# Kernel tuning notes

Measured on AMD Instinct MI355X. Metric: run time of the kernel, lower is better.

The kernel has to match this reference:

```python
import jax, jax.numpy as jnp
import numpy as np

B, S, HIDDEN, NH = 2, 2048, 1024, 16
D = HIDDEN // NH  # 64
PHYS_W, CONS_W = 0.2, 0.15
LN_EPS = 1e-5


def _layernorm(x, gamma, beta):
    mu = jnp.mean(x, axis=-1, keepdims=True)
    var = jnp.mean(jnp.square(x - mu), axis=-1, keepdims=True)
    return (x - mu) * jax.lax.rsqrt(var + LN_EPS) * gamma + beta


def setup_inputs() -> dict:
    key = jax.random.key(0)
    ks = jax.random.split(key, 12)
    s = 0.02
    return {
        "cnn_features": jax.random.normal(ks[0], (B, S, HIDDEN), jnp.float32),
        "llm_features": jax.random.normal(ks[1], (B, S, HIDDEN), jnp.float32),
        # Linear weights stored [in, out] so y = x @ W + b (torch's W.T)
        "Wq": jax.random.normal(ks[2], (HIDDEN, HIDDEN), jnp.float32) * s,
        "bq": jnp.zeros((HIDDEN,), jnp.float32),
        "Wk": jax.random.normal(ks[3], (HIDDEN, HIDDEN), jnp.float32) * s,
        "bk": jnp.zeros((HIDDEN,), jnp.float32),
        "Wv": jax.random.normal(ks[4], (HIDDEN, HIDDEN), jnp.float32) * s,
        "bv": jnp.zeros((HIDDEN,), jnp.float32),
        "Wo": jax.random.normal(ks[5], (HIDDEN, HIDDEN), jnp.float32) * s,
        "bo": jnp.zeros((HIDDEN,), jnp.float32),
        "energy_emb": jax.random.normal(ks[6], (1, 1, HIDDEN), jnp.float32),
        "mass_emb": jax.random.normal(ks[7], (1, 1, HIDDEN), jnp.float32),
        "momentum_emb": jax.random.normal(ks[8], (1, 1, HIDDEN), jnp.float32),
        "gamma": jnp.ones((HIDDEN,), jnp.float32),
        "beta": jnp.zeros((HIDDEN,), jnp.float32),
    }


def reference(cnn_features, llm_features, Wq, bq, Wk, bk, Wv, bv, Wo, bo,
              energy_emb, mass_emb, momentum_emb, gamma, beta):
    Bsz, Sc, _ = cnn_features.shape
    Sl = llm_features.shape[1]

    def attn(q_in, kv_in):
        Sq, Sk = q_in.shape[1], kv_in.shape[1]
        Q = (q_in @ Wq + bq).reshape(Bsz, Sq, NH, D).transpose(0, 2, 1, 3)   # bhqd
        K = (kv_in @ Wk + bk).reshape(Bsz, Sk, NH, D).transpose(0, 2, 1, 3)  # bhkd
        V = (kv_in @ Wv + bv).reshape(Bsz, Sk, NH, D).transpose(0, 2, 1, 3)  # bhkd
        scores = jnp.einsum('bhqd,bhkd->bhqk', Q, K) / np.float32(np.sqrt(D))
        # physics biases: require Sq == Sk (elementwise Q*K), shape [B,H,Sq,1]
        energy_bias = jnp.sum(Q * K, axis=-1, keepdims=True) * PHYS_W
        mass_bias = jnp.mean(Q + K, axis=-1, keepdims=True) * CONS_W
        attn_w = jax.nn.softmax(scores + energy_bias + mass_bias, axis=-1)
        attended = jnp.einsum('bhqk,bhkd->bhqd', attn_w, V)
        attended = attended.transpose(0, 2, 1, 3).reshape(Bsz, Sq, HIDDEN)
        out = attended @ Wo + bo
        return _layernorm(q_in + out, gamma, beta)

    phys = jnp.concatenate([
        jnp.broadcast_to(energy_emb, (Bsz, 1, HIDDEN)),
        jnp.broadcast_to(mass_emb, (Bsz, 1, HIDDEN)),
        jnp.broadcast_to(momentum_emb, (Bsz, 1, HIDDEN)),
    ], axis=1)  # [B, 3, HIDDEN]
    aug_cnn = jnp.concatenate([cnn_features, phys], axis=1)  # [B, Sc+3, H]
    aug_llm = jnp.concatenate([llm_features, phys], axis=1)  # [B, Sl+3, H]

    cnn_att = attn(aug_cnn, aug_llm)
    llm_att = attn(aug_llm, aug_cnn)
    return cnn_att[:, :Sc, :], llm_att[:, :Sl, :]
```

## Files before the change

### kernel.cpp

```cpp
#include <hip/hip_runtime.h>

#define BN 2
#define SS 2048
#define SA 2051
#define HID 1024
#define NHD 16
#define DH 64
#define GSTR 40
#define VTLD 8320
#define KSTR 72
#define VSTR 40
#define MFMA16 __builtin_amdgcn_mfma_f32_16x16x32_bf16
#define QSCALE 0.18033688011112042f

typedef __attribute__((ext_vector_type(4))) float floatx4;
typedef __attribute__((ext_vector_type(8))) short bf16x8;
typedef __attribute__((ext_vector_type(2))) unsigned uintx2;

__device__ __forceinline__ float bf2f(short s) {
  union { unsigned u; float f; } v; v.u = ((unsigned)(unsigned short)s) << 16; return v.f;
}
__device__ __forceinline__ short f2bf(float f) {
  union { float f; unsigned u; } v; v.f = f;
  unsigned u = v.u;
  u += 0x7FFF + ((u >> 16) & 1);
  return (short)(u >> 16);
}
__device__ __forceinline__ unsigned pack2(float lo, float hi) {
  unsigned ul = __float_as_uint(lo) + 0x8000u;
  unsigned uh = __float_as_uint(hi) + 0x8000u;
  return __builtin_amdgcn_perm(uh, ul, 0x07060302u);
}
__device__ __forceinline__ unsigned cvtpk(float lo, float hi) {
  unsigned r;
  asm("v_cvt_pk_bf16_f32 %0, %1, %2" : "=v"(r) : "v"(lo), "v"(hi));
  return r;
}
__device__ __forceinline__ uintx2 qtrans(unsigned A, unsigned B) {
  auto t = __builtin_amdgcn_permlane32_swap(A, B, false, false);
  auto u = __builtin_amdgcn_permlane16_swap(t[0], t[1], false, false);
  uintx2 r; r[0] = u[0]; r[1] = u[1];
  return r;
}
__device__ __forceinline__ bool in_is_f32(const unsigned* graw) {
  return graw[0] == 0x3F800000u;
}

__global__ __launch_bounds__(256) void convert_in(const void* __restrict__ src, long off,
                                                  short* __restrict__ dst, int n,
                                                  const unsigned* __restrict__ graw) {
  bool f32 = in_is_f32(graw);
  int i = (blockIdx.x * 256 + threadIdx.x) * 4;
  int stride = gridDim.x * 1024;
  if (f32) {
    const float* s = (const float*)src + off;
    for (; i < n; i += stride) {
      float4 v = *(const float4*)(s + i);
      short4 o; o.x = f2bf(v.x); o.y = f2bf(v.y); o.z = f2bf(v.z); o.w = f2bf(v.w);
      *(short4*)(dst + i) = o;
    }
  } else {
    const short* s = (const short*)src + off;
    for (; i < n; i += stride)
      *(short4*)(dst + i) = *(const short4*)(s + i);
  }
}

__global__ __launch_bounds__(256) void convert_small(
    const void* s0, const void* s1, const void* s2, const void* s3,
    const void* s4, const void* s5, const void* s6, const void* s7,
    const void* s8, short* __restrict__ dst, const unsigned* __restrict__ graw) {
  bool f32 = in_is_f32(graw);
  const void* srcs[9] = {s0, s1, s2, s3, s4, s5, s6, s7, s8};
  const void* s = srcs[blockIdx.x];
  short* d = dst + (size_t)blockIdx.x * 1024;
  for (int i = threadIdx.x; i < 1024; i += 256)
    d[i] = f32 ? f2bf(((const float*)s)[i]) : ((const short*)s)[i];
}

__global__ __launch_bounds__(256) void conv_wt(const void* __restrict__ W,
    short* __restrict__ WT, const unsigned* __restrict__ graw) {
  __shared__ short tile[32][33];
  bool f32 = in_is_f32(graw);
  int n0 = blockIdx.x * 32, k0 = blockIdx.y * 32;
  int tx = threadIdx.x & 31, ty = threadIdx.x >> 5;
#pragma unroll
  for (int i = 0; i < 4; i++) {
    int k = k0 + ty + i*8;
    short v = f32 ? f2bf(((const float*)W)[(size_t)k * HID + n0 + tx])
                  : ((const short*)W)[(size_t)k * HID + n0 + tx];
    tile[ty + i*8][tx] = v;
  }
  __syncthreads();
#pragma unroll
  for (int i = 0; i < 4; i++)
    WT[(size_t)(n0 + ty + i*8) * HID + k0 + tx] = tile[tx][ty + i*8];
}

__global__ __launch_bounds__(256) void gemm_bf(
    const short* __restrict__ A, int tailA,
    const short* __restrict__ B, int tailB,
    const short* __restrict__ embB,
    const short* __restrict__ bias, int bias_row, float scale,
    short* __restrict__ out16, float* __restrict__ out32, long ldc,
    const void* __restrict__ rc0, const void* __restrict__ rc1,
    const unsigned* __restrict__ graw) {
  __shared__ __align__(16) short sA[128 * GSTR];
  __shared__ __align__(16) short sB[128 * GSTR];
  int t = threadIdx.x;
  int wave = t >> 6, lane = t & 63, l16 = lane & 15, quad = lane >> 4;
  int m0 = blockIdx.y * 128, n0 = blockIdx.x * 128;
  int msub = (wave >> 1) * 64, nsub = (wave & 1) * 64;

  floatx4 acc[4][4] = {};
  for (int k0 = 0; k0 < HID; k0 += 32) {
    bf16x8 av[2], bv2[2];
#pragma unroll
    for (int rep = 0; rep < 2; rep++) {
      int cid = rep * 256 + t;
      int row = cid >> 2, kc = (cid & 3) * 8;
      int ra = m0 + row;
      const short* ap;
      if (tailA && ra >= 8192) ap = embB + (size_t)((ra > 8194 ? 8194 : ra) - 8192) * 1024;
      else                     ap = A + (size_t)ra * HID;
      av[rep] = *(const bf16x8*)(ap + k0 + kc);
      int rb = n0 + row;
      const short* bp;
      if (tailB && rb >= 8192) bp = embB + (size_t)((rb > 8194 ? 8194 : rb) - 8192) * 1024;
      else                     bp = B + (size_t)rb * HID;
      bv2[rep] = *(const bf16x8*)(bp + k0 + kc);
    }
    __syncthreads();
#pragma unroll
    for (int rep = 0; rep < 2; rep++) {
      int cid = rep * 256 + t;
      int row = cid >> 2, kc = (cid & 3) * 8;
      *(bf16x8*)(&sA[row * GSTR + kc]) = av[rep];
      *(bf16x8*)(&sB[row * GSTR + kc]) = bv2[rep];
    }
    __syncthreads();
    bf16x8 af[4], bf_[4];
#pragma unroll
    for (int i = 0; i < 4; i++) {
      af[i]  = *(const bf16x8*)(&sA[(msub + i*16 + l16) * GSTR + quad*8]);
      bf_[i] = *(const bf16x8*)(&sB[(nsub + i*16 + l16) * GSTR + quad*8]);
    }
#pragma unroll
    for (int mi = 0; mi < 4; mi++)
#pragma unroll
      for (int ni = 0; ni < 4; ni++)
        acc[mi][ni] = MFMA16(af[mi], bf_[ni], acc[mi][ni], 0, 0, 0);
  }

  bool f32in = in_is_f32(graw);
#pragma unroll
  for (int mi = 0; mi < 4; mi++)
#pragma unroll
    for (int ni = 0; ni < 4; ni++) {
      int col = n0 + nsub + ni*16 + l16;
      float bcol = bias_row ? 0.f : bf2f(bias[col]);
#pragma unroll
      for (int r = 0; r < 4; r++) {
        int m = m0 + msub + mi*16 + quad*4 + r;
        float v = (acc[mi][ni][r] + (bias_row ? bf2f(bias[m]) : bcol)) * scale;
        if (out32) {
          float res;
          if (f32in) res = ((const float*)(m < 4096 ? rc0 : rc1))[(size_t)(m & 4095) * HID + col];
          else       res = bf2f(((const short*)(m < 4096 ? rc0 : rc1))[(size_t)(m & 4095) * HID + col]);
          out32[(size_t)m * HID + col] = v + res;
        } else {
          out16[(size_t)m * ldc + col] = f2bf(v);
        }
      }
    }
}

__global__ __launch_bounds__(256, 4) void flash3(
    const short* __restrict__ Qa, const short* __restrict__ Ka,
    const short* __restrict__ VTa, short* __restrict__ att) {
  __shared__ __align__(16) short sK0[32*KSTR], sK1[32*KSTR];
  __shared__ __align__(16) short sV0[64*VSTR], sV1[64*VSTR];
  int t = threadIdx.x, wave = t >> 6, lane = t & 63;
  int l16 = lane & 15, quad = lane >> 4;
  int bid = blockIdx.x;
  int swz = (bid & 7) * 128 + (bid >> 3);
  int qt  = swz & 15;
  int h   = (swz >> 4) & 15;
  int sb  = swz >> 8;
  int side = sb >> 1, b = sb & 1;
  int qrow0 = side * 4096 + b * 2048;
  int kvb = (side ^ 1) * 4096 + b * 2048;
  int q0 = qt * 128 + wave * 32;

  const short* qp0 = Qa + (size_t)(qrow0 + q0 + l16) * HID + h*DH + quad*8;
  const short* qp1 = qp0 + 16 * HID;
  bf16x8 qa0 = *(const bf16x8*)qp0, qb0 = *(const bf16x8*)(qp0 + 32);
  bf16x8 qa1 = *(const bf16x8*)qp1, qb1 = *(const bf16x8*)(qp1 + 32);

  float rs0 = 0.f, rs1 = 0.f;
  floatx4 oA[4] = {}, oB[4] = {};

  int krow = t >> 3, kc8 = (t & 7) * 8;
  int vrow = t >> 2, vc8 = (t & 3) * 8;
  const short* kgp = Ka + (size_t)(kvb + krow) * HID + h*DH + kc8;
  const short* vgp = VTa + (size_t)(h*DH + vrow) * VTLD + kvb + vc8;
  bf16x8 kreg = *(const bf16x8*)kgp;
  bf16x8 vreg = *(const bf16x8*)vgp;
  short *kw = sK0, *vw = sV0, *ka = sK1, *va = sV1;

  for (int kv0 = 0; kv0 < 2048; kv0 += 32) {
    *(bf16x8*)(kw + krow*KSTR + kc8) = kreg;
    *(bf16x8*)(vw + vrow*VSTR + vc8) = vreg;
    __syncthreads();
    kgp += 32*HID; vgp += 32;
    kreg = *(const bf16x8*)kgp;
    vreg = *(const bf16x8*)vgp;

    bf16x8 k00 = *(const bf16x8*)(kw + l16*KSTR + quad*8);
    bf16x8 k01 = *(const bf16x8*)(kw + l16*KSTR + 32 + quad*8);
    bf16x8 k10 = *(const bf16x8*)(kw + (16 + l16)*KSTR + quad*8);
    bf16x8 k11 = *(const bf16x8*)(kw + (16 + l16)*KSTR + 32 + quad*8);
    bf16x8 v0 = *(const bf16x8*)(vw + l16*VSTR + quad*8);
    bf16x8 v1 = *(const bf16x8*)(vw + (16 + l16)*VSTR + quad*8);
    bf16x8 v2 = *(const bf16x8*)(vw + (32 + l16)*VSTR + quad*8);
    bf16x8 v3 = *(const bf16x8*)(vw + (48 + l16)*VSTR + quad*8);

    floatx4 s00 = {}, s10 = {}, s01 = {}, s11 = {};
    s00 = MFMA16(k00, qa0, s00, 0, 0, 0); s00 = MFMA16(k01, qb0, s00, 0, 0, 0);
    s10 = MFMA16(k10, qa0, s10, 0, 0, 0); s10 = MFMA16(k11, qb0, s10, 0, 0, 0);
    s01 = MFMA16(k00, qa1, s01, 0, 0, 0); s01 = MFMA16(k01, qb1, s01, 0, 0, 0);
    s11 = MFMA16(k10, qa1, s11, 0, 0, 0); s11 = MFMA16(k11, qb1, s11, 0, 0, 0);

    floatx4 p00, p10, p01, p11;
#pragma unroll
    for (int r = 0; r < 4; r++) {
      p00[r] = exp2f(s00[r]); p10[r] = exp2f(s10[r]);
      p01[r] = exp2f(s01[r]); p11[r] = exp2f(s11[r]);
    }
    rs0 += ((p00[0]+p00[1])+(p00[2]+p00[3])) + ((p10[0]+p10[1])+(p10[2]+p10[3]));
    rs1 += ((p01[0]+p01[1])+(p01[2]+p01[3])) + ((p11[0]+p11[1])+(p11[2]+p11[3]));

    unsigned pc00 = cvtpk(p00[0], p00[1]), pc01 = cvtpk(p00[2], p00[3]);
    unsigned pc10 = cvtpk(p10[0], p10[1]), pc11 = cvtpk(p10[2], p10[3]);
    unsigned pd00 = cvtpk(p01[0], p01[1]), pd01 = cvtpk(p01[2], p01[3]);
    unsigned pd10 = cvtpk(p11[0], p11[1]), pd11 = cvtpk(p11[2], p11[3]);
    uintx2 uA0 = qtrans(pc00, pc10);
    uintx2 uA1 = qtrans(pc01, pc11);
    uintx2 uB0 = qtrans(pd00, pd10);
    uintx2 uB1 = qtrans(pd01, pd11);
    union { unsigned u[4]; bf16x8 v; } pf0, pf1;
    pf0.u[0] = uA0[0]; pf0.u[1] = uA1[0]; pf0.u[2] = uA0[1]; pf0.u[3] = uA1[1];
    pf1.u[0] = uB0[0]; pf1.u[1] = uB1[0]; pf1.u[2] = uB0[1]; pf1.u[3] = uB1[1];

    oA[0] = MFMA16(v0, pf0.v, oA[0], 0, 0, 0);
    oA[1] = MFMA16(v1, pf0.v, oA[1], 0, 0, 0);
    oA[2] = MFMA16(v2, pf0.v, oA[2], 0, 0, 0);
    oA[3] = MFMA16(v3, pf0.v, oA[3], 0, 0, 0);
    oB[0] = MFMA16(v0, pf1.v, oB[0], 0, 0, 0);
    oB[1] = MFMA16(v1, pf1.v, oB[1], 0, 0, 0);
    oB[2] = MFMA16(v2, pf1.v, oB[2], 0, 0, 0);
    oB[3] = MFMA16(v3, pf1.v, oB[3], 0, 0, 0);

    short* tk = kw; kw = ka; ka = tk;
    short* tv = vw; vw = va; va = tv;
  }

  {
    int er = l16 < 2 ? l16 : 2;
    const short* kpt = Ka + (size_t)(8192 + er) * HID + h*DH + quad*8;
    bf16x8 tk0 = *(const bf16x8*)kpt;
    bf16x8 tk1 = *(const bf16x8*)(kpt + 32);
    floatx4 s00 = {}, s01 = {};
    s00 = MFMA16(tk0, qa0, s00, 0, 0, 0); s00 = MFMA16(tk1, qb0, s00, 0, 0, 0);
    s01 = MFMA16(tk0, qa1, s01, 0, 0, 0); s01 = MFMA16(tk1, qb1, s01, 0, 0, 0);
    floatx4 p00, p01;
#pragma unroll
    for (int r = 0; r < 4; r++) {
      bool val = (quad == 0) && (r < 3);
      p00[r] = val ? exp2f(s00[r]) : 0.f;
      p01[r] = val ? exp2f(s01[r]) : 0.f;
    }
    rs0 += (p00[0]+p00[1]) + (p00[2]+p00[3]);
    rs1 += (p01[0]+p01[1]) + (p01[2]+p01[3]);
    unsigned pc00 = cvtpk(p00[0], p00[1]), pc01 = cvtpk(p00[2], p00[3]);
    unsigned pd00 = cvtpk(p01[0], p01[1]), pd01 = cvtpk(p01[2], p01[3]);
    uintx2 uA0 = qtrans(pc00, 0u);
    uintx2 uA1 = qtrans(pc01, 0u);
    uintx2 uB0 = qtrans(pd00, 0u);
    uintx2 uB1 = qtrans(pd01, 0u);
    union { unsigned u[4]; bf16x8 v; } pf0, pf1;
    pf0.u[0] = uA0[0]; pf0.u[1] = uA1[0]; pf0.u[2] = uA0[1]; pf0.u[3] = uA1[1];
    pf1.u[0] = uB0[0]; pf1.u[1] = uB1[0]; pf1.u[2] = uB0[1]; pf1.u[3] = uB1[1];
    const short* vtp = VTa + (size_t)(h*DH + l16) * VTLD + 8192 + quad*8;
    bf16x8 v0 = *(const bf16x8*)vtp;
    bf16x8 v1 = *(const bf16x8*)(vtp + 16*VTLD);
    bf16x8 v2 = *(const bf16x8*)(vtp + 32*VTLD);
    bf16x8 v3 = *(const bf16x8*)(vtp + 48*VTLD);
    oA[0] = MFMA16(v0, pf0.v, oA[0], 0, 0, 0);
    oA[1] = MFMA16(v1, pf0.v, oA[1], 0, 0, 0);
    oA[2] = MFMA16(v2, pf0.v, oA[2], 0, 0, 0);
    oA[3] = MFMA16(v3, pf0.v, oA[3], 0, 0, 0);
    oB[0] = MFMA16(v0, pf1.v, oB[0], 0, 0, 0);
    oB[1] = MFMA16(v1, pf1.v, oB[1], 0, 0, 0);
    oB[2] = MFMA16(v2, pf1.v, oB[2], 0, 0, 0);
    oB[3] = MFMA16(v3, pf1.v, oB[3], 0, 0, 0);
  }

  rs0 += __shfl_xor(rs0, 16, 64); rs0 += __shfl_xor(rs0, 32, 64);
  rs1 += __shfl_xor(rs1, 16, 64); rs1 += __shfl_xor(rs1, 32, 64);
  float i0 = 1.f / rs0, i1 = 1.f / rs1;

  unsigned* ob0 = (unsigned*)(att + (size_t)(qrow0 + q0 + l16) * HID + h*DH + quad*4);
  unsigned* ob1 = (unsigned*)(att + (size_t)(qrow0 + q0 + 16 + l16) * HID + h*DH + quad*4);
#pragma unroll
  for (int n = 0; n < 4; n++) {
    ob0[n*8]     = pack2(oA[n][0]*i0, oA[n][1]*i0);
    ob0[n*8 + 1] = pack2(oA[n][2]*i0, oA[n][3]*i0);
    ob1[n*8]     = pack2(oB[n][0]*i1, oB[n][1]*i1);
    ob1[n*8 + 1] = pack2(oB[n][2]*i1, oB[n][3]*i1);
  }
}

__global__ __launch_bounds__(256) void ln_kernel(
    const float* __restrict__ y, const short* __restrict__ gamma,
    const short* __restrict__ beta, void* __restrict__ outp, long orow,
    const unsigned* __restrict__ graw) {
  bool f32o = in_is_f32(graw);
  int row = blockIdx.x;
  int t = threadIdx.x;
  const float* yr = y + (size_t)row * HID;
  float4 v = ((const float4*)yr)[t];
  float sum = v.x + v.y + v.z + v.w;
#pragma unroll
  for (int off = 32; off >= 1; off >>= 1) sum += __shfl_xor(sum, off, 64);
  __shared__ float red[8];
  int wave = t >> 6, lane = t & 63;
  if (lane == 0) red[wave] = sum;
  __syncthreads();
  float mu = (red[0] + red[1] + red[2] + red[3]) * (1.f/HID);
  float dx = v.x - mu, dy = v.y - mu, dz = v.z - mu, dw = v.w - mu;
  float sq = dx*dx + dy*dy + dz*dz + dw*dw;
#pragma unroll
  for (int off = 32; off >= 1; off >>= 1) sq += __shfl_xor(sq, off, 64);
  if (lane == 0) red[4 + wave] = sq;
  __syncthreads();
  float var = (red[4] + red[5] + red[6] + red[7]) * (1.f/HID);
  float inv = rsqrtf(var + 1e-5f);
  const short* g = gamma + t*4;
  const short* be = beta + t*4;
  float o0 = dx * inv * bf2f(g[0]) + bf2f(be[0]);
  float o1 = dy * inv * bf2f(g[1]) + bf2f(be[1]);
  float o2 = dz * inv * bf2f(g[2]) + bf2f(be[2]);
  float o3 = dw * inv * bf2f(g[3]) + bf2f(be[3]);
  size_t base = (size_t)(orow + row) * HID + t*4;
  if (f32o) {
    float4 ov = {o0, o1, o2, o3};
    *(float4*)((float*)outp + base) = ov;
  } else {
    short4 ov = {f2bf(o0), f2bf(o1), f2bf(o2), f2bf(o3)};
    *(short4*)((short*)outp + base) = ov;
  }
}

extern "C" void kernel_launch(void* const* d_in, const int* in_sizes, int n_in,
                              void* d_out, int out_size, void* d_ws, size_t ws_size,
                              hipStream_t stream) {
  const void* cnn = d_in[0];
  const void* llm = d_in[1];
  const void* Wq  = d_in[2];
  const void* bq  = d_in[3];
  const void* Wk  = d_in[4];
  const void* bk  = d_in[5];
  const void* Wv  = d_in[6];
  const void* bv  = d_in[7];
  const void* Wo  = d_in[8];
  const void* bo  = d_in[9];
  const void* ee  = d_in[10];
  const void* me  = d_in[11];
  const void* pe  = d_in[12];
  const void* gamma = d_in[13];
  const void* beta  = d_in[14];
  const unsigned* graw = (const unsigned*)gamma;
  (void)in_sizes; (void)n_in; (void)out_size; (void)ws_size;

  char* p = (char*)d_ws;
  auto alloc = [&](size_t bytes) { char* r = p; p += (bytes + 255) & ~(size_t)255; return r; };
  short* WqT = (short*)alloc((size_t)HID*HID*2);
  short* WkT = (short*)alloc((size_t)HID*HID*2);
  short* WvT = (short*)alloc((size_t)HID*HID*2);
  short* WoT = (short*)alloc((size_t)HID*HID*2);
  short* smallB = (short*)alloc(9 * 1024 * 2);
  short* Qa  = (short*)alloc((size_t)8192 * HID * 2);
  short* Ka  = (short*)alloc((size_t)8320 * HID * 2);
  short* VT  = (short*)alloc((size_t)HID * VTLD * 2);
  float* y   = (float*)Qa;
  short* att = (short*)d_out;
  short* Xa  = (short*)d_out + (size_t)8192 * HID;
  short* bqB = smallB;        short* bkB = smallB + 1024;
  short* bvB = smallB + 2048; short* boB = smallB + 3072;
  short* embB = smallB + 4096;
  short* gB  = smallB + 7168; short* bB  = smallB + 8192;

  dim3 tb(256);
  dim3 tg(32, 32);
  const int NF = 4096 * HID;

  convert_in<<<dim3(NF/1024), tb, 0, stream>>>(cnn, 0, Xa, NF, graw);
  convert_in<<<dim3(NF/1024), tb, 0, stream>>>(llm, 0, Xa + (size_t)NF, NF, graw);
  conv_wt<<<tg, tb, 0, stream>>>(Wq, WqT, graw);
  conv_wt<<<tg, tb, 0, stream>>>(Wk, WkT, graw);
  conv_wt<<<tg, tb, 0, stream>>>(Wv, WvT, graw);
  conv_wt<<<tg, tb, 0, stream>>>(Wo, WoT, graw);
  convert_small<<<dim3(9), tb, 0, stream>>>(bq, bk, bv, bo, ee, me, pe, gamma, beta,
                                            smallB, graw);

  gemm_bf<<<dim3(8, 64), tb, 0, stream>>>(Xa, 0, WqT, 0, embB, bqB, 0, QSCALE,
      Qa, nullptr, HID, cnn, llm, graw);
  gemm_bf<<<dim3(8, 65), tb, 0, stream>>>(Xa, 1, WkT, 0, embB, bkB, 0, 1.f,
      Ka, nullptr, HID, cnn, llm, graw);
  gemm_bf<<<dim3(65, 8), tb, 0, stream>>>(WvT, 0, Xa, 1, embB, bvB, 1, 1.f,
      VT, nullptr, VTLD, cnn, llm, graw);

  flash3<<<dim3(1024), tb, 0, stream>>>(Qa, Ka, VT, att);

  gemm_bf<<<dim3(8, 64), tb, 0, stream>>>(att, 0, WoT, 0, embB, boB, 0, 1.f,
      nullptr, y, HID, cnn, llm, graw);

  ln_kernel<<<dim3(8192), tb, 0, stream>>>(y, gB, bB, d_out, 0, graw);
}
```

Baseline: 434.0 us.

## Stage GEMM tiles with direct global-to-LDS loads, swizzle blocks, fast exp2, MFMA priority

The projection GEMM now loads its A/B tiles with global_load_lds straight into unpadded shared memory, which removes the register round trip, and prefetches the next k-slice after fragments are read. Workgroup ids are swizzled across 8 groups so neighbouring blocks share cache lines. The attention kernel uses the hardware v_exp_f32 instruction in place of exp2f and raises wave priority around its MFMA blocks. Together these aim to cut GEMM load latency and attention ALU overhead. Dropping the LDS padding (GSTR 40→32) can bring bank conflicts on fragment reads, and the fast exp gives up denormal and range handling.

```diff
diff --git a/kernel.cpp b/kernel.cpp
--- a/kernel.cpp
+++ b/kernel.cpp
@@ -6,7 +6,7 @@
 #define HID 1024
 #define NHD 16
 #define DH 64
-#define GSTR 40
+#define GSTR 32
 #define VTLD 8320
 #define KSTR 72
 #define VSTR 40
@@ -36,11 +36,23 @@
   asm("v_cvt_pk_bf16_f32 %0, %1, %2" : "=v"(r) : "v"(lo), "v"(hi));
   return r;
 }
+__device__ __forceinline__ float exp2fast(float x) {
+#if __has_builtin(__builtin_amdgcn_exp2f)
+  return __builtin_amdgcn_exp2f(x);
+#else
+  float r; asm("v_exp_f32 %0, %1" : "=v"(r) : "v"(x)); return r;
+#endif
+}
 __device__ __forceinline__ uintx2 qtrans(unsigned A, unsigned B) {
   auto t = __builtin_amdgcn_permlane32_swap(A, B, false, false);
   auto u = __builtin_amdgcn_permlane16_swap(t[0], t[1], false, false);
   uintx2 r; r[0] = u[0]; r[1] = u[1];
   return r;
+}
+__device__ __forceinline__ void gload16(const short* g, short* l) {
+  __builtin_amdgcn_global_load_lds(
+      (const __attribute__((address_space(1))) void*)g,
+      (__attribute__((address_space(3))) void*)l, 16, 0, 0);
 }
 __device__ __forceinline__ bool in_is_f32(const unsigned* graw) {
   return graw[0] == 0x3F800000u;
@@ -109,41 +121,53 @@
   __shared__ __align__(16) short sB[128 * GSTR];
   int t = threadIdx.x;
   int wave = t >> 6, lane = t & 63, l16 = lane & 15, quad = lane >> 4;
-  int m0 = blockIdx.y * 128, n0 = blockIdx.x * 128;
+  int nwg = gridDim.x * gridDim.y;
+  int bid = blockIdx.y * gridDim.x + blockIdx.x;
+  int cpx = nwg >> 3;
+  int swz = (bid & 7) * cpx + (bid >> 3);
+  int bx = swz % gridDim.x, by = swz / gridDim.x;
+  int m0 = by * 128, n0 = bx * 128;
   int msub = (wave >> 1) * 64, nsub = (wave & 1) * 64;
+
+  const short* apr[2]; const short* bpr[2]; short* ldA[2]; short* ldB[2];
+#pragma unroll
+  for (int rep = 0; rep < 2; rep++) {
+    int cid = rep * 256 + t;
+    int row = cid >> 2, kc = (cid & 3) * 8;
+    int ra = m0 + row;
+    const short* ap;
+    if (tailA && ra >= 8192) ap = embB + (size_t)((ra > 8194 ? 8194 : ra) - 8192) * 1024;
+    else                     ap = A + (size_t)ra * HID;
+    int rb = n0 + row;
+    const short* bp;
+    if (tailB && rb >= 8192) bp = embB + (size_t)((rb > 8194 ? 8194 : rb) - 8192) * 1024;
+    else                     bp = B + (size_t)rb * HID;
+    apr[rep] = ap + kc; bpr[rep] = bp + kc;
+    ldA[rep] = &sA[(rep*256 + wave*64) * 8];
+    ldB[rep] = &sB[(rep*256 + wave*64) * 8];
+  }
+#pragma unroll
+  for (int rep = 0; rep < 2; rep++) {
+    gload16(apr[rep], ldA[rep]);
+    gload16(bpr[rep], ldB[rep]);
+  }
 
   floatx4 acc[4][4] = {};
   for (int k0 = 0; k0 < HID; k0 += 32) {
-    bf16x8 av[2], bv2[2];
-#pragma unroll
-    for (int rep = 0; rep < 2; rep++) {
-      int cid = rep * 256 + t;
-      int row = cid >> 2, kc = (cid & 3) * 8;
-      int ra = m0 + row;
-      const short* ap;
-      if (tailA && ra >= 8192) ap = embB + (size_t)((ra > 8194 ? 8194 : ra) - 8192) * 1024;
-      else                     ap = A + (size_t)ra * HID;
-      av[rep] = *(const bf16x8*)(ap + k0 + kc);
-      int rb = n0 + row;
-      const short* bp;
-      if (tailB && rb >= 8192) bp = embB + (size_t)((rb > 8194 ? 8194 : rb) - 8192) * 1024;
-      else                     bp = B + (size_t)rb * HID;
-      bv2[rep] = *(const bf16x8*)(bp + k0 + kc);
-    }
-    __syncthreads();
-#pragma unroll
-    for (int rep = 0; rep < 2; rep++) {
-      int cid = rep * 256 + t;
-      int row = cid >> 2, kc = (cid & 3) * 8;
-      *(bf16x8*)(&sA[row * GSTR + kc]) = av[rep];
-      *(bf16x8*)(&sB[row * GSTR + kc]) = bv2[rep];
-    }
     __syncthreads();
     bf16x8 af[4], bf_[4];
 #pragma unroll
     for (int i = 0; i < 4; i++) {
       af[i]  = *(const bf16x8*)(&sA[(msub + i*16 + l16) * GSTR + quad*8]);
       bf_[i] = *(const bf16x8*)(&sB[(nsub + i*16 + l16) * GSTR + quad*8]);
+    }
+    __syncthreads();
+    if (k0 + 32 < HID) {
+#pragma unroll
+      for (int rep = 0; rep < 2; rep++) {
+        gload16(apr[rep] + k0 + 32, ldA[rep]);
+        gload16(bpr[rep] + k0 + 32, ldB[rep]);
+      }
     }
 #pragma unroll
     for (int mi = 0; mi < 4; mi++)
@@ -226,16 +250,18 @@
     bf16x8 v3 = *(const bf16x8*)(vw + (48 + l16)*VSTR + quad*8);
 
     floatx4 s00 = {}, s10 = {}, s01 = {}, s11 = {};
+    __builtin_amdgcn_s_setprio(1);
     s00 = MFMA16(k00, qa0, s00, 0, 0, 0); s00 = MFMA16(k01, qb0, s00, 0, 0, 0);
     s10 = MFMA16(k10, qa0, s10, 0, 0, 0); s10 = MFMA16(k11, qb0, s10, 0, 0, 0);
     s01 = MFMA16(k00, qa1, s01, 0, 0, 0); s01 = MFMA16(k01, qb1, s01, 0, 0, 0);
     s11 = MFMA16(k10, qa1, s11, 0, 0, 0); s11 = MFMA16(k11, qb1, s11, 0, 0, 0);
+    __builtin_amdgcn_s_setprio(0);
 
     floatx4 p00, p10, p01, p11;
 #pragma unroll
     for (int r = 0; r < 4; r++) {
-      p00[r] = exp2f(s00[r]); p10[r] = exp2f(s10[r]);
-      p01[r] = exp2f(s01[r]); p11[r] = exp2f(s11[r]);
+      p00[r] = exp2fast(s00[r]); p10[r] = exp2fast(s10[r]);
+      p01[r] = exp2fast(s01[r]); p11[r] = exp2fast(s11[r]);
     }
     rs0 += ((p00[0]+p00[1])+(p00[2]+p00[3])) + ((p10[0]+p10[1])+(p10[2]+p10[3]));
     rs1 += ((p01[0]+p01[1])+(p01[2]+p01[3])) + ((p11[0]+p11[1])+(p11[2]+p11[3]));
@@ -252,6 +278,7 @@
     pf0.u[0] = uA0[0]; pf0.u[1] = uA1[0]; pf0.u[2] = uA0[1]; pf0.u[3] = uA1[1];
     pf1.u[0] = uB0[0]; pf1.u[1] = uB1[0]; pf1.u[2] = uB0[1]; pf1.u[3] = uB1[1];
 
+    __builtin_amdgcn_s_setprio(1);
     oA[0] = MFMA16(v0, pf0.v, oA[0], 0, 0, 0);
     oA[1] = MFMA16(v1, pf0.v, oA[1], 0, 0, 0);
     oA[2] = MFMA16(v2, pf0.v, oA[2], 0, 0, 0);
@@ -260,6 +287,7 @@
     oB[1] = MFMA16(v1, pf1.v, oB[1], 0, 0, 0);
     oB[2] = MFMA16(v2, pf1.v, oB[2], 0, 0, 0);
     oB[3] = MFMA16(v3, pf1.v, oB[3], 0, 0, 0);
+    __builtin_amdgcn_s_setprio(0);
 
     short* tk = kw; kw = ka; ka = tk;
     short* tv = vw; vw = va; va = tv;
@@ -277,8 +305,8 @@
 #pragma unroll
     for (int r = 0; r < 4; r++) {
       bool val = (quad == 0) && (r < 3);
-      p00[r] = val ? exp2f(s00[r]) : 0.f;
-      p01[r] = val ? exp2f(s01[r]) : 0.f;
+      p00[r] = val ? exp2fast(s00[r]) : 0.f;
+      p01[r] = val ? exp2fast(s01[r]) : 0.f;
     }
     rs0 += (p00[0]+p00[1]) + (p00[2]+p00[3]);
     rs1 += (p01[0]+p01[1]) + (p01[2]+p01[3]);
```

Result: faster. 384.8 us (-11.3%).
